# Performance work log

Measured on AMD Instinct MI355X. Metric: run time of the kernel, lower is better.

Reference implementation:

```python
import jax, jax.numpy as jnp
import numpy as np

X_DIM, R_DIM, U_DIM, V_DIM, H_DIM = 64, 64, 64, 64, 128


def setup_inputs() -> dict:
    key = jax.random.key(0)
    k1, k2, k3, k4, k5 = jax.random.split(key, 5)
    n, i, j = 8, 32, 32
    r = jax.random.normal(k1, (n, i, j, R_DIM), dtype=jnp.float32)
    u = jax.random.normal(k2, (n, R_DIM, U_DIM, V_DIM), dtype=jnp.float32)
    v = jax.random.normal(k3, (n, i, j, V_DIM), dtype=jnp.float32)
    # xavier_uniform scaling: gain=1, fan computed over last two dims per torch default
    def xavier(k, shape):
        fan_in, fan_out = shape[-1], shape[-2]
        # torch xavier on >2D tensor: fan_in = shape[1]*prod(shape[2:]), fan_out = shape[0]*prod(shape[2:])
        rf = int(np.prod(shape[2:])) if len(shape) > 2 else 1
        fi = shape[1] * rf
        fo = shape[0] * rf
        bound = float(np.sqrt(6.0 / (fi + fo)))
        return jax.random.uniform(k, shape, dtype=jnp.float32, minval=-bound, maxval=bound)
    w1 = xavier(k4, (R_DIM, U_DIM, V_DIM, H_DIM))
    w2 = xavier(k5, (X_DIM, R_DIM, H_DIM))
    return {"r": r, "u": u, "v": v, "w1": w1, "w2": w2}


def reference(r, u, v, w1, w2):
    # contract w1 with u over (u_dim, v_dim) -> per-batch tensor a[n, r, v', h]
    # original: einsum('ruvh,nruv,nijv->nijrh')
    a = jnp.einsum('ruvh,nruv->nrvh', w1, u)          # contract u axis; v survives? no:
    # Careful: in 'ruvh,nruv,nijv->nijrh', v is contracted across all three.
    # Do it in two GEMM-friendly steps: first contract u-axis, keeping v.
    # a: [n, r, v, h] (contracted only over u)
    a = jnp.einsum('ruvh,nruv->nrvh', w1, u)
    # then contract v with v-tensor: [n,i,j,v] x [n,r,v,h] -> [n,i,j,r,h]
    x = jax.nn.relu(jnp.einsum('nijv,nrvh->nijrh', v, a))
    # second einsum: 'xrh,nijr,nijrh->nijx'
    # fuse r-weighting into x first (elementwise over r), then contract (r,h) with w2
    out = jnp.einsum('xrh,nijrh->nijx', w2, x * r[..., None])
    return out
```

## Files before the change

kernel.cpp:

```cpp
#include <hip/hip_runtime.h>
#include <hip/hip_bf16.h>

#define RD 64
#define UD 64
#define VD 64
#define HD 128
#define XD 64
#define NB 8
#define SITES 1024

typedef float f32x4 __attribute__((ext_vector_type(4)));
typedef __bf16 bf16x4 __attribute__((ext_vector_type(4)));
typedef __bf16 bf16x8 __attribute__((ext_vector_type(8)));
typedef unsigned int u32x4 __attribute__((ext_vector_type(4)));
typedef unsigned short u16;
typedef unsigned short u16x4 __attribute__((ext_vector_type(4)));

__global__ void kprep(const float* __restrict__ w2, u16* __restrict__ w2t,
                      const float* __restrict__ r, float* __restrict__ rt,
                      const float* __restrict__ u, float* __restrict__ ut) {
  __shared__ float tl[64][68];
  int b = blockIdx.x;
  int t = threadIdx.x;
  if (b < 256) {
    int rr = b >> 2, qq = b & 3;
    for (int i = 0; i < 8; ++i) {
      int idx = qq * 2048 + i * 256 + t;
      int x = idx >> 7, h = idx & 127;
      float val = w2[((size_t)x * RD + rr) * HD + h];
      __hip_bfloat16 hv = __float2bfloat16(val);
      w2t[((size_t)rr * XD + x) * HD + h] = *(u16*)&hv;
    }
  } else if (b < 384) {
    int bb = b - 256;
    int n = bb >> 4, sb = (bb & 15) * 64;
    for (int i = 0; i < 4; ++i) {
      int flat = i * 256 + t;
      int s = flat >> 4, ch = flat & 15;
      f32x4 d = *(const f32x4*)(r + ((size_t)(n * SITES + sb + s) * RD + ch * 4));
      *(f32x4*)&tl[s][ch * 4] = d;
    }
    __syncthreads();
    for (int i = 0; i < 4; ++i) {
      int flat = i * 256 + t;
      int rr = flat >> 4, ch = flat & 15;
      f32x4 o;
      o.x = tl[ch * 4 + 0][rr];
      o.y = tl[ch * 4 + 1][rr];
      o.z = tl[ch * 4 + 2][rr];
      o.w = tl[ch * 4 + 3][rr];
      *(f32x4*)(rt + ((size_t)(n * RD + rr) * SITES + sb + ch * 4)) = o;
    }
  } else {
    int f = (b - 384) * 256 + t;
    int nh = f & 1, v = (f >> 1) & 63, uu = (f >> 7) & 63, rr = f >> 13;
    f32x4 o;
#pragma unroll
    for (int k = 0; k < 4; ++k)
      o[k] = u[(((size_t)(nh * 4 + k) * RD + rr) * UD + uu) * VD + v];
    *(f32x4*)(ut + (size_t)f * 4) = o;
  }
}

__global__ __launch_bounds__(256, 4) void k_a(const float* __restrict__ w1,
                                              const float* __restrict__ ut,
                                              float* __restrict__ part) {
  __shared__ float tile[32][34];
  int b = blockIdx.x;
  int rr = b >> 4, uh = (b >> 3) & 1, vh = (b >> 2) & 1, hb = b & 3;
  int t = threadIdx.x;
  int vl = t >> 3, hs = t & 7;
  int v = vh * 32 + vl;
  int h0 = hb * 32 + hs * 4;
  const float* w1p = w1 + ((size_t)((rr * UD) + uh * 32) * VD + v) * HD + h0;
  const float* up  = ut + ((size_t)((rr * UD) + uh * 32) * VD + v) * NB;

  float acc[8][4];
#pragma unroll
  for (int n = 0; n < 8; ++n)
#pragma unroll
    for (int j = 0; j < 4; ++j) acc[n][j] = 0.f;

#pragma unroll 4
  for (int uu = 0; uu < 32; ++uu) {
    f32x4 wv = *(const f32x4*)(w1p + (size_t)uu * (VD * HD));
    f32x4 a0 = *(const f32x4*)(up + (size_t)uu * (VD * NB));
    f32x4 a1 = *(const f32x4*)(up + (size_t)uu * (VD * NB) + 4);
    float un[8];
    un[0] = a0.x; un[1] = a0.y; un[2] = a0.z; un[3] = a0.w;
    un[4] = a1.x; un[5] = a1.y; un[6] = a1.z; un[7] = a1.w;
#pragma unroll
    for (int n = 0; n < 8; ++n)
#pragma unroll
      for (int j = 0; j < 4; ++j) acc[n][j] += un[n] * wv[j];
  }

  int hl = t >> 3, vs = t & 7;
  float* pb = part + (size_t)uh * (NB * RD * HD * VD);
  for (int n = 0; n < 8; ++n) {
    __syncthreads();
#pragma unroll
    for (int j = 0; j < 4; ++j) tile[hs * 4 + j][vl] = acc[n][j];
    __syncthreads();
    f32x4 blk = *(const f32x4*)&tile[hl][vs * 4];
    *(f32x4*)(pb + ((size_t)(n * RD + rr) * HD + hb * 32 + hl) * VD + vh * 32 + vs * 4) = blk;
  }
}

__global__ __launch_bounds__(256) void k_a_red(const float* __restrict__ part,
                                               u16* __restrict__ at) {
  int i0 = blockIdx.x * 256 + threadIdx.x;
  const float* p1 = part + (size_t)NB * RD * HD * VD;
#pragma unroll
  for (int k = 0; k < 4; ++k) {
    size_t i = ((size_t)i0 + (size_t)k * 262144) * 4;
    f32x4 a = *(const f32x4*)(part + i);
    f32x4 c = *(const f32x4*)(p1 + i);
    u16x4 o;
#pragma unroll
    for (int j = 0; j < 4; ++j) {
      __hip_bfloat16 hv = __float2bfloat16(a[j] + c[j]);
      o[j] = *(u16*)&hv;
    }
    *(u16x4*)(at + i) = o;
  }
}

__global__ __launch_bounds__(256, 1) void k_main(const float* __restrict__ vin,
                                                 const u16* __restrict__ at,
                                                 const u16* __restrict__ w2t,
                                                 const float* __restrict__ rt,
                                                 float* __restrict__ pbuf) {
  __shared__ __align__(16) char Plds[2 * 128 * 256];
  int b = blockIdx.x;
  int rc = b & 7, st = (b >> 3) & 7, n = b >> 6;
  int t = threadIdx.x;
  int w = t >> 6, L = t & 63, q = L >> 4, c = L & 15;
  int g1m = w >> 1, g1n = w & 1;
  int g2m = w >> 1, g2x = w & 1;

  bf16x8 vf[4][2];
#pragma unroll
  for (int nt = 0; nt < 4; ++nt)
#pragma unroll
    for (int ks = 0; ks < 2; ++ks) {
      int s = g1n * 64 + nt * 16 + c;
      const float* vp = vin + ((size_t)(n * SITES + st * 128 + s) * VD + ks * 32 + q * 8);
      f32x4 a0 = *(const f32x4*)vp;
      f32x4 a1 = *(const f32x4*)(vp + 4);
      bf16x8 f;
      f[0] = (__bf16)a0.x; f[1] = (__bf16)a0.y; f[2] = (__bf16)a0.z; f[3] = (__bf16)a0.w;
      f[4] = (__bf16)a1.x; f[5] = (__bf16)a1.y; f[6] = (__bf16)a1.z; f[7] = (__bf16)a1.w;
      vf[nt][ks] = f;
    }

  f32x4 o[4][2];
#pragma unroll
  for (int i = 0; i < 4; i++)
#pragma unroll
    for (int j = 0; j < 2; j++) o[i][j] = (f32x4)0.f;

  for (int rr = rc * 8; rr < rc * 8 + 8; ++rr) {
    const u16* abase = at + (size_t)(n * RD + rr) * 8192;

    bf16x8 af[4][2];
#pragma unroll
    for (int mt = 0; mt < 4; ++mt)
#pragma unroll
      for (int ks = 0; ks < 2; ++ks) {
        int h = g1m * 64 + mt * 16 + c;
        int vb = ks * 4 + q;
        af[mt][ks] = *(const bf16x8*)(abase + (size_t)h * VD + vb * 8);
      }
    u32x4 wraw[2][4];
#pragma unroll
    for (int xt = 0; xt < 2; ++xt)
#pragma unroll
      for (int k2 = 0; k2 < 4; ++k2) {
        int xg = g2x * 32 + xt * 16 + c;
        wraw[xt][k2] = *(const u32x4*)((const char*)w2t +
                        (((size_t)(rr * XD + xg)) * HD + k2 * 32 + q * 8) * 2);
      }
    float rsc[4];
#pragma unroll
    for (int nt = 0; nt < 4; ++nt)
      rsc[nt] = rt[(size_t)(n * RD + rr) * SITES + st * 128 + g1n * 64 + nt * 16 + c];

    f32x4 cc[4][4];
#pragma unroll
    for (int mt = 0; mt < 4; ++mt)
#pragma unroll
      for (int nt = 0; nt < 4; ++nt) cc[mt][nt] = (f32x4)0.f;
#pragma unroll
    for (int ks = 0; ks < 2; ++ks)
#pragma unroll
      for (int mt = 0; mt < 4; ++mt)
#pragma unroll
        for (int nt = 0; nt < 4; ++nt)
          cc[mt][nt] = __builtin_amdgcn_mfma_f32_16x16x32_bf16(af[mt][ks], vf[nt][ks],
                                                               cc[mt][nt], 0, 0, 0);

    char* PB = Plds + (rr & 1) * 32768;
#pragma unroll
    for (int mt = 0; mt < 4; ++mt)
#pragma unroll
      for (int nt = 0; nt < 4; ++nt) {
        float sc = rsc[nt];
        bf16x4 pv;
#pragma unroll
        for (int jj = 0; jj < 4; ++jj) {
          float x = cc[mt][nt][jj];
          x = x > 0.f ? x : 0.f;
          pv[jj] = (__bf16)(x * sc);
        }
        int s = g1n * 64 + nt * 16 + c;
        int blk = g1m * 8 + mt * 2 + (q >> 1);
        *(bf16x4*)(PB + (size_t)s * 256 + (size_t)((blk ^ c) * 16 + (q & 1) * 8)) = pv;
      }
    __syncthreads();

#pragma unroll
    for (int k2 = 0; k2 < 4; ++k2) {
      bf16x8 wf0 = __builtin_bit_cast(bf16x8, wraw[0][k2]);
      bf16x8 wf1 = __builtin_bit_cast(bf16x8, wraw[1][k2]);
#pragma unroll
      for (int mt = 0; mt < 4; ++mt) {
        int s = g2m * 64 + mt * 16 + c;
        int blk = k2 * 4 + q;
        bf16x8 pf = *(const bf16x8*)(PB + (size_t)s * 256 + (size_t)((blk ^ c) * 16));
        o[mt][0] = __builtin_amdgcn_mfma_f32_16x16x32_bf16(pf, wf0, o[mt][0], 0, 0, 0);
        o[mt][1] = __builtin_amdgcn_mfma_f32_16x16x32_bf16(pf, wf1, o[mt][1], 0, 0, 0);
      }
    }
  }
#pragma unroll
  for (int mt = 0; mt < 4; ++mt)
#pragma unroll
    for (int xt = 0; xt < 2; ++xt) {
      int s0 = g2m * 64 + mt * 16 + q * 4;
      int x = g2x * 32 + xt * 16 + c;
      size_t off = ((((size_t)rc * NB + n) * 8 + st) * XD + x) * 128 + s0;
      *(f32x4*)(pbuf + off) = o[mt][xt];
    }
}

__global__ __launch_bounds__(256) void k_reduce(const float* __restrict__ pbuf,
                                                float* __restrict__ out) {
  __shared__ float tile[128][17];
  int b = blockIdx.x;
  int n = b >> 5, st = (b >> 2) & 7, xq = b & 3;
  int t = threadIdx.x;
  int sq = t & 31, xl = t >> 5;
#pragma unroll
  for (int p = 0; p < 2; ++p) {
    int x = xq * 16 + p * 8 + xl;
    f32x4 sum = (f32x4)0.f;
#pragma unroll
    for (int rcc = 0; rcc < 8; ++rcc) {
      size_t off = ((((size_t)rcc * NB + n) * 8 + st) * XD + x) * 128 + sq * 4;
      f32x4 d = *(const f32x4*)(pbuf + off);
      sum.x += d.x; sum.y += d.y; sum.z += d.z; sum.w += d.w;
    }
#pragma unroll
    for (int k = 0; k < 4; ++k) tile[sq * 4 + k][p * 8 + xl] = sum[k];
  }
  __syncthreads();
#pragma unroll
  for (int k = 0; k < 2; ++k) {
    int flat = k * 256 + t;
    int s = flat >> 2, c4 = flat & 3;
    f32x4 o;
#pragma unroll
    for (int j = 0; j < 4; ++j) o[j] = tile[s][c4 * 4 + j];
    *(f32x4*)(out + ((size_t)(n * SITES + st * 128 + s) * XD + xq * 16 + c4 * 4)) = o;
  }
}

extern "C" void kernel_launch(void* const* d_in, const int* in_sizes, int n_in,
                              void* d_out, int out_size, void* d_ws, size_t ws_size,
                              hipStream_t stream) {
  const float* r  = (const float*)d_in[0];
  const float* u  = (const float*)d_in[1];
  const float* v  = (const float*)d_in[2];
  const float* w1 = (const float*)d_in[3];
  const float* w2 = (const float*)d_in[4];
  float* out = (float*)d_out;
  char* ws = (char*)d_ws;
  u16* at     = (u16*)(ws);
  u16* w2t    = (u16*)(ws + ((size_t)8 << 20));
  float* rt   = (float*)(ws + ((size_t)9 << 20));
  float* ut   = (float*)(ws + ((size_t)11 << 20));
  float* part = (float*)(ws + ((size_t)19 << 20));
  float* pbuf = (float*)(ws + ((size_t)51 << 20));

  hipLaunchKernelGGL(kprep, dim3(2432), dim3(256), 0, stream, w2, w2t, r, rt, u, ut);
  hipLaunchKernelGGL(k_a, dim3(1024), dim3(256), 0, stream, w1, ut, part);
  hipLaunchKernelGGL(k_a_red, dim3(1024), dim3(256), 0, stream, part, at);
  hipLaunchKernelGGL(k_main, dim3(512), dim3(256), 0, stream, v, at, w2t, rt, pbuf);
  hipLaunchKernelGGL(k_reduce, dim3(256), dim3(256), 0, stream, pbuf, out);
}
```

Measured before the change: 270.9 us.

## Drop split-U partial reduction in k_a and halve k_main site tile

```diff
diff --git a/kernel.cpp b/kernel.cpp
--- a/kernel.cpp
+++ b/kernel.cpp
@@ -14,7 +14,6 @@
 typedef __bf16 bf16x8 __attribute__((ext_vector_type(8)));
 typedef unsigned int u32x4 __attribute__((ext_vector_type(4)));
 typedef unsigned short u16;
-typedef unsigned short u16x4 __attribute__((ext_vector_type(4)));
 
 __global__ void kprep(const float* __restrict__ w2, u16* __restrict__ w2t,
                       const float* __restrict__ r, float* __restrict__ rt,
@@ -64,79 +63,61 @@
 
 __global__ __launch_bounds__(256, 4) void k_a(const float* __restrict__ w1,
                                               const float* __restrict__ ut,
-                                              float* __restrict__ part) {
-  __shared__ float tile[32][34];
-  int b = blockIdx.x;
-  int rr = b >> 4, uh = (b >> 3) & 1, vh = (b >> 2) & 1, hb = b & 3;
+                                              u16* __restrict__ at) {
+  __shared__ u16 tile[16][36];
+  int b = blockIdx.x;
+  int rr = b >> 4, vh = (b >> 3) & 1, hb = b & 7;
   int t = threadIdx.x;
   int vl = t >> 3, hs = t & 7;
   int v = vh * 32 + vl;
-  int h0 = hb * 32 + hs * 4;
-  const float* w1p = w1 + ((size_t)((rr * UD) + uh * 32) * VD + v) * HD + h0;
-  const float* up  = ut + ((size_t)((rr * UD) + uh * 32) * VD + v) * NB;
-
-  float acc[8][4];
-#pragma unroll
-  for (int n = 0; n < 8; ++n)
-#pragma unroll
-    for (int j = 0; j < 4; ++j) acc[n][j] = 0.f;
+  int h0 = hb * 16 + hs * 2;
+  const float* w1p = w1 + ((size_t)(rr * UD) * VD + v) * HD + h0;
+  const float* up  = ut + ((size_t)(rr * UD) * VD + v) * NB;
+
+  float acc[8][2];
+#pragma unroll
+  for (int n = 0; n < 8; ++n) { acc[n][0] = 0.f; acc[n][1] = 0.f; }
 
 #pragma unroll 4
-  for (int uu = 0; uu < 32; ++uu) {
-    f32x4 wv = *(const f32x4*)(w1p + (size_t)uu * (VD * HD));
+  for (int uu = 0; uu < 64; ++uu) {
+    float2 wv = *(const float2*)(w1p + (size_t)uu * (VD * HD));
     f32x4 a0 = *(const f32x4*)(up + (size_t)uu * (VD * NB));
     f32x4 a1 = *(const f32x4*)(up + (size_t)uu * (VD * NB) + 4);
     float un[8];
     un[0] = a0.x; un[1] = a0.y; un[2] = a0.z; un[3] = a0.w;
     un[4] = a1.x; un[5] = a1.y; un[6] = a1.z; un[7] = a1.w;
 #pragma unroll
-    for (int n = 0; n < 8; ++n)
-#pragma unroll
-      for (int j = 0; j < 4; ++j) acc[n][j] += un[n] * wv[j];
-  }
-
-  int hl = t >> 3, vs = t & 7;
-  float* pb = part + (size_t)uh * (NB * RD * HD * VD);
+    for (int n = 0; n < 8; ++n) {
+      acc[n][0] += un[n] * wv.x;
+      acc[n][1] += un[n] * wv.y;
+    }
+  }
+
+  int hl = t >> 4, vs = t & 15;
   for (int n = 0; n < 8; ++n) {
     __syncthreads();
 #pragma unroll
-    for (int j = 0; j < 4; ++j) tile[hs * 4 + j][vl] = acc[n][j];
-    __syncthreads();
-    f32x4 blk = *(const f32x4*)&tile[hl][vs * 4];
-    *(f32x4*)(pb + ((size_t)(n * RD + rr) * HD + hb * 32 + hl) * VD + vh * 32 + vs * 4) = blk;
-  }
-}
-
-__global__ __launch_bounds__(256) void k_a_red(const float* __restrict__ part,
-                                               u16* __restrict__ at) {
-  int i0 = blockIdx.x * 256 + threadIdx.x;
-  const float* p1 = part + (size_t)NB * RD * HD * VD;
-#pragma unroll
-  for (int k = 0; k < 4; ++k) {
-    size_t i = ((size_t)i0 + (size_t)k * 262144) * 4;
-    f32x4 a = *(const f32x4*)(part + i);
-    f32x4 c = *(const f32x4*)(p1 + i);
-    u16x4 o;
-#pragma unroll
-    for (int j = 0; j < 4; ++j) {
-      __hip_bfloat16 hv = __float2bfloat16(a[j] + c[j]);
-      o[j] = *(u16*)&hv;
-    }
-    *(u16x4*)(at + i) = o;
-  }
-}
-
-__global__ __launch_bounds__(256, 1) void k_main(const float* __restrict__ vin,
+    for (int j = 0; j < 2; ++j) {
+      __hip_bfloat16 hv = __float2bfloat16(acc[n][j]);
+      tile[hs * 2 + j][vl] = *(u16*)&hv;
+    }
+    __syncthreads();
+    unsigned int blk = *(const unsigned int*)&tile[hl][vs * 2];
+    *(unsigned int*)(at + ((size_t)(n * RD + rr) * HD + hb * 16 + hl) * VD +
+                     vh * 32 + vs * 2) = blk;
+  }
+}
+
+__global__ __launch_bounds__(256, 3) void k_main(const float* __restrict__ vin,
                                                  const u16* __restrict__ at,
                                                  const u16* __restrict__ w2t,
                                                  const float* __restrict__ rt,
                                                  float* __restrict__ pbuf) {
-  __shared__ __align__(16) char Plds[2 * 128 * 256];
-  int b = blockIdx.x;
-  int rc = b & 7, st = (b >> 3) & 7, n = b >> 6;
+  __shared__ __align__(16) char Plds[2 * 64 * 256];
+  int b = blockIdx.x;
+  int rc = b & 7, st = (b >> 3) & 15, n = b >> 7;
   int t = threadIdx.x;
   int w = t >> 6, L = t & 63, q = L >> 4, c = L & 15;
-  int g1m = w >> 1, g1n = w & 1;
   int g2m = w >> 1, g2x = w & 1;
 
   bf16x8 vf[4][2];
@@ -144,8 +125,8 @@
   for (int nt = 0; nt < 4; ++nt)
 #pragma unroll
     for (int ks = 0; ks < 2; ++ks) {
-      int s = g1n * 64 + nt * 16 + c;
-      const float* vp = vin + ((size_t)(n * SITES + st * 128 + s) * VD + ks * 32 + q * 8);
+      int s = nt * 16 + c;
+      const float* vp = vin + ((size_t)(n * SITES + st * 64 + s) * VD + ks * 32 + q * 8);
       f32x4 a0 = *(const f32x4*)vp;
       f32x4 a1 = *(const f32x4*)(vp + 4);
       bf16x8 f;
@@ -154,55 +135,55 @@
       vf[nt][ks] = f;
     }
 
-  f32x4 o[4][2];
-#pragma unroll
-  for (int i = 0; i < 4; i++)
+  f32x4 o[2][2];
+#pragma unroll
+  for (int i = 0; i < 2; i++)
 #pragma unroll
     for (int j = 0; j < 2; j++) o[i][j] = (f32x4)0.f;
 
   for (int rr = rc * 8; rr < rc * 8 + 8; ++rr) {
     const u16* abase = at + (size_t)(n * RD + rr) * 8192;
 
-    bf16x8 af[4][2];
-#pragma unroll
-    for (int mt = 0; mt < 4; ++mt)
+    bf16x8 af[2][2];
+#pragma unroll
+    for (int mt = 0; mt < 2; ++mt)
 #pragma unroll
       for (int ks = 0; ks < 2; ++ks) {
-        int h = g1m * 64 + mt * 16 + c;
+        int h = w * 32 + mt * 16 + c;
         int vb = ks * 4 + q;
         af[mt][ks] = *(const bf16x8*)(abase + (size_t)h * VD + vb * 8);
       }
     u32x4 wraw[2][4];
 #pragma unroll
-    for (int xt = 0; xt < 2; ++xt)
+    for (int nt = 0; nt < 2; ++nt)
 #pragma unroll
       for (int k2 = 0; k2 < 4; ++k2) {
-        int xg = g2x * 32 + xt * 16 + c;
-        wraw[xt][k2] = *(const u32x4*)((const char*)w2t +
+        int xg = g2x * 32 + nt * 16 + c;
+        wraw[nt][k2] = *(const u32x4*)((const char*)w2t +
                         (((size_t)(rr * XD + xg)) * HD + k2 * 32 + q * 8) * 2);
       }
     float rsc[4];
 #pragma unroll
     for (int nt = 0; nt < 4; ++nt)
-      rsc[nt] = rt[(size_t)(n * RD + rr) * SITES + st * 128 + g1n * 64 + nt * 16 + c];
-
-    f32x4 cc[4][4];
-#pragma unroll
-    for (int mt = 0; mt < 4; ++mt)
+      rsc[nt] = rt[(size_t)(n * RD + rr) * SITES + st * 64 + nt * 16 + c];
+
+    f32x4 cc[2][4];
+#pragma unroll
+    for (int mt = 0; mt < 2; ++mt)
 #pragma unroll
       for (int nt = 0; nt < 4; ++nt) cc[mt][nt] = (f32x4)0.f;
 #pragma unroll
     for (int ks = 0; ks < 2; ++ks)
 #pragma unroll
-      for (int mt = 0; mt < 4; ++mt)
+      for (int mt = 0; mt < 2; ++mt)
 #pragma unroll
         for (int nt = 0; nt < 4; ++nt)
           cc[mt][nt] = __builtin_amdgcn_mfma_f32_16x16x32_bf16(af[mt][ks], vf[nt][ks],
                                                                cc[mt][nt], 0, 0, 0);
 
-    char* PB = Plds + (rr & 1) * 32768;
-#pragma unroll
-    for (int mt = 0; mt < 4; ++mt)
+    char* PB = Plds + (rr & 1) * 16384;
+#pragma unroll
+    for (int mt = 0; mt < 2; ++mt)
 #pragma unroll
       for (int nt = 0; nt < 4; ++nt) {
         float sc = rsc[nt];
@@ -213,8 +194,8 @@
           x = x > 0.f ? x : 0.f;
           pv[jj] = (__bf16)(x * sc);
         }
-        int s = g1n * 64 + nt * 16 + c;
-        int blk = g1m * 8 + mt * 2 + (q >> 1);
+        int s = nt * 16 + c;
+        int blk = w * 4 + mt * 2 + (q >> 1);
         *(bf16x4*)(PB + (size_t)s * 256 + (size_t)((blk ^ c) * 16 + (q & 1) * 8)) = pv;
       }
     __syncthreads();
@@ -224,8 +205,8 @@
       bf16x8 wf0 = __builtin_bit_cast(bf16x8, wraw[0][k2]);
       bf16x8 wf1 = __builtin_bit_cast(bf16x8, wraw[1][k2]);
 #pragma unroll
-      for (int mt = 0; mt < 4; ++mt) {
-        int s = g2m * 64 + mt * 16 + c;
+      for (int mt = 0; mt < 2; ++mt) {
+        int s = g2m * 32 + mt * 16 + c;
         int blk = k2 * 4 + q;
         bf16x8 pf = *(const bf16x8*)(PB + (size_t)s * 256 + (size_t)((blk ^ c) * 16));
         o[mt][0] = __builtin_amdgcn_mfma_f32_16x16x32_bf16(pf, wf0, o[mt][0], 0, 0, 0);
@@ -234,45 +215,45 @@
     }
   }
 #pragma unroll
-  for (int mt = 0; mt < 4; ++mt)
-#pragma unroll
-    for (int xt = 0; xt < 2; ++xt) {
-      int s0 = g2m * 64 + mt * 16 + q * 4;
-      int x = g2x * 32 + xt * 16 + c;
-      size_t off = ((((size_t)rc * NB + n) * 8 + st) * XD + x) * 128 + s0;
-      *(f32x4*)(pbuf + off) = o[mt][xt];
+  for (int mt = 0; mt < 2; ++mt)
+#pragma unroll
+    for (int nt = 0; nt < 2; ++nt) {
+      int s0 = g2m * 32 + mt * 16 + q * 4;
+      int x = g2x * 32 + nt * 16 + c;
+      size_t off = ((((size_t)rc * NB + n) * 16 + st) * XD + x) * 64 + s0;
+      *(f32x4*)(pbuf + off) = o[mt][nt];
     }
 }
 
 __global__ __launch_bounds__(256) void k_reduce(const float* __restrict__ pbuf,
                                                 float* __restrict__ out) {
-  __shared__ float tile[128][17];
-  int b = blockIdx.x;
-  int n = b >> 5, st = (b >> 2) & 7, xq = b & 3;
-  int t = threadIdx.x;
-  int sq = t & 31, xl = t >> 5;
-#pragma unroll
-  for (int p = 0; p < 2; ++p) {
-    int x = xq * 16 + p * 8 + xl;
+  __shared__ float tile[64][68];
+  int b = blockIdx.x;
+  int n = b >> 4, st = b & 15;
+  int t = threadIdx.x;
+  int sq = t & 15, xl = t >> 4;
+#pragma unroll
+  for (int p = 0; p < 4; ++p) {
+    int x = p * 16 + xl;
     f32x4 sum = (f32x4)0.f;
 #pragma unroll
     for (int rcc = 0; rcc < 8; ++rcc) {
-      size_t off = ((((size_t)rcc * NB + n) * 8 + st) * XD + x) * 128 + sq * 4;
+      size_t off = ((((size_t)rcc * NB + n) * 16 + st) * XD + x) * 64 + sq * 4;
       f32x4 d = *(const f32x4*)(pbuf + off);
       sum.x += d.x; sum.y += d.y; sum.z += d.z; sum.w += d.w;
     }
 #pragma unroll
-    for (int k = 0; k < 4; ++k) tile[sq * 4 + k][p * 8 + xl] = sum[k];
+    for (int k = 0; k < 4; ++k) tile[sq * 4 + k][x] = sum[k];
   }
   __syncthreads();
 #pragma unroll
-  for (int k = 0; k < 2; ++k) {
+  for (int k = 0; k < 4; ++k) {
     int flat = k * 256 + t;
-    int s = flat >> 2, c4 = flat & 3;
+    int s = flat >> 4, c4 = flat & 15;
     f32x4 o;
 #pragma unroll
     for (int j = 0; j < 4; ++j) o[j] = tile[s][c4 * 4 + j];
-    *(f32x4*)(out + ((size_t)(n * SITES + st * 128 + s) * XD + xq * 16 + c4 * 4)) = o;
+    *(f32x4*)(out + ((size_t)(n * SITES + st * 64 + s) * XD + c4 * 4)) = o;
   }
 }
 
@@ -290,12 +271,10 @@
   u16* w2t    = (u16*)(ws + ((size_t)8 << 20));
   float* rt   = (float*)(ws + ((size_t)9 << 20));
   float* ut   = (float*)(ws + ((size_t)11 << 20));
-  float* part = (float*)(ws + ((size_t)19 << 20));
-  float* pbuf = (float*)(ws + ((size_t)51 << 20));
+  float* pbuf = (float*)(ws + ((size_t)19 << 20));
 
   hipLaunchKernelGGL(kprep, dim3(2432), dim3(256), 0, stream, w2, w2t, r, rt, u, ut);
-  hipLaunchKernelGGL(k_a, dim3(1024), dim3(256), 0, stream, w1, ut, part);
-  hipLaunchKernelGGL(k_a_red, dim3(1024), dim3(256), 0, stream, part, at);
-  hipLaunchKernelGGL(k_main, dim3(512), dim3(256), 0, stream, v, at, w2t, rt, pbuf);
-  hipLaunchKernelGGL(k_reduce, dim3(256), dim3(256), 0, stream, pbuf, out);
-}
+  hipLaunchKernelGGL(k_a, dim3(1024), dim3(256), 0, stream, w1, ut, at);
+  hipLaunchKernelGGL(k_main, dim3(1024), dim3(256), 0, stream, v, at, w2t, rt, pbuf);
+  hipLaunchKernelGGL(k_reduce, dim3(128), dim3(256), 0, stream, pbuf, out);
+}
```

Measured after the change: 287.2 us. 6.0% more time.

## Keep GEMM1 output in registers as GEMM2 operand via permuted w2 layout

Applied to the files above, without the earlier changes.

```diff
diff --git a/kernel.cpp b/kernel.cpp
--- a/kernel.cpp
+++ b/kernel.cpp
@@ -16,7 +16,7 @@
 typedef unsigned short u16;
 typedef unsigned short u16x4 __attribute__((ext_vector_type(4)));
 
-__global__ void kprep(const float* __restrict__ w2, u16* __restrict__ w2t,
+__global__ void kprep(const float* __restrict__ w2, u16* __restrict__ w2p,
                       const float* __restrict__ r, float* __restrict__ rt,
                       const float* __restrict__ u, float* __restrict__ ut) {
   __shared__ float tl[64][68];
@@ -26,10 +26,12 @@
     int rr = b >> 2, qq = b & 3;
     for (int i = 0; i < 8; ++i) {
       int idx = qq * 2048 + i * 256 + t;
-      int x = idx >> 7, h = idx & 127;
-      float val = w2[((size_t)x * RD + rr) * HD + h];
+      int x = idx >> 7, pos = idx & 127;
+      int k2 = pos >> 5, qd = (pos >> 3) & 3, jhi = (pos >> 2) & 1, jl = pos & 3;
+      int hsrc = k2 * 32 + jhi * 16 + qd * 4 + jl;
+      float val = w2[((size_t)x * RD + rr) * HD + hsrc];
       __hip_bfloat16 hv = __float2bfloat16(val);
-      w2t[((size_t)rr * XD + x) * HD + h] = *(u16*)&hv;
+      w2p[((size_t)rr * XD + x) * HD + pos] = *(u16*)&hv;
     }
   } else if (b < 384) {
     int bb = b - 256;
@@ -126,26 +128,23 @@
   }
 }
 
-__global__ __launch_bounds__(256, 1) void k_main(const float* __restrict__ vin,
-                                                 const u16* __restrict__ at,
-                                                 const u16* __restrict__ w2t,
-                                                 const float* __restrict__ rt,
-                                                 float* __restrict__ pbuf) {
-  __shared__ __align__(16) char Plds[2 * 128 * 256];
-  int b = blockIdx.x;
-  int rc = b & 7, st = (b >> 3) & 7, n = b >> 6;
-  int t = threadIdx.x;
-  int w = t >> 6, L = t & 63, q = L >> 4, c = L & 15;
-  int g1m = w >> 1, g1n = w & 1;
-  int g2m = w >> 1, g2x = w & 1;
-
-  bf16x8 vf[4][2];
-#pragma unroll
-  for (int nt = 0; nt < 4; ++nt)
+__global__ __launch_bounds__(64, 2) void k_main(const float* __restrict__ vin,
+                                                const u16* __restrict__ at,
+                                                const u16* __restrict__ w2p,
+                                                const float* __restrict__ rt,
+                                                float* __restrict__ pbuf) {
+  int b = blockIdx.x;
+  int stile = b & 31, rc = (b >> 5) & 7, n = b >> 8;
+  int t = threadIdx.x;
+  int q = t >> 4, c = t & 15;
+
+  bf16x8 vf[2][2];
+#pragma unroll
+  for (int nt = 0; nt < 2; ++nt)
 #pragma unroll
     for (int ks = 0; ks < 2; ++ks) {
-      int s = g1n * 64 + nt * 16 + c;
-      const float* vp = vin + ((size_t)(n * SITES + st * 128 + s) * VD + ks * 32 + q * 8);
+      const float* vp = vin + ((size_t)(n * SITES + stile * 32 + nt * 16 + c) * VD +
+                               ks * 32 + q * 8);
       f32x4 a0 = *(const f32x4*)vp;
       f32x4 a1 = *(const f32x4*)(vp + 4);
       bf16x8 f;
@@ -154,125 +153,120 @@
       vf[nt][ks] = f;
     }
 
-  f32x4 o[4][2];
-#pragma unroll
-  for (int i = 0; i < 4; i++)
-#pragma unroll
-    for (int j = 0; j < 2; j++) o[i][j] = (f32x4)0.f;
+  f32x4 o[2][4];
+#pragma unroll
+  for (int i = 0; i < 2; ++i)
+#pragma unroll
+    for (int j = 0; j < 4; ++j) o[i][j] = (f32x4)0.f;
 
   for (int rr = rc * 8; rr < rc * 8 + 8; ++rr) {
     const u16* abase = at + (size_t)(n * RD + rr) * 8192;
 
-    bf16x8 af[4][2];
-#pragma unroll
-    for (int mt = 0; mt < 4; ++mt)
-#pragma unroll
-      for (int ks = 0; ks < 2; ++ks) {
-        int h = g1m * 64 + mt * 16 + c;
-        int vb = ks * 4 + q;
-        af[mt][ks] = *(const bf16x8*)(abase + (size_t)h * VD + vb * 8);
-      }
-    u32x4 wraw[2][4];
-#pragma unroll
-    for (int xt = 0; xt < 2; ++xt)
-#pragma unroll
-      for (int k2 = 0; k2 < 4; ++k2) {
-        int xg = g2x * 32 + xt * 16 + c;
-        wraw[xt][k2] = *(const u32x4*)((const char*)w2t +
-                        (((size_t)(rr * XD + xg)) * HD + k2 * 32 + q * 8) * 2);
-      }
-    float rsc[4];
-#pragma unroll
-    for (int nt = 0; nt < 4; ++nt)
-      rsc[nt] = rt[(size_t)(n * RD + rr) * SITES + st * 128 + g1n * 64 + nt * 16 + c];
-
-    f32x4 cc[4][4];
-#pragma unroll
-    for (int mt = 0; mt < 4; ++mt)
-#pragma unroll
-      for (int nt = 0; nt < 4; ++nt) cc[mt][nt] = (f32x4)0.f;
+    bf16x8 af[8][2];
+#pragma unroll
+    for (int mt = 0; mt < 8; ++mt)
+#pragma unroll
+      for (int ks = 0; ks < 2; ++ks)
+        af[mt][ks] = *(const bf16x8*)(abase + (size_t)(mt * 16 + c) * VD +
+                                      (ks * 4 + q) * 8);
+    float rsc[2];
+#pragma unroll
+    for (int nt = 0; nt < 2; ++nt)
+      rsc[nt] = rt[(size_t)(n * RD + rr) * SITES + stile * 32 + nt * 16 + c];
+
+    f32x4 cc[8][2];
+#pragma unroll
+    for (int mt = 0; mt < 8; ++mt)
+#pragma unroll
+      for (int nt = 0; nt < 2; ++nt) cc[mt][nt] = (f32x4)0.f;
 #pragma unroll
     for (int ks = 0; ks < 2; ++ks)
 #pragma unroll
-      for (int mt = 0; mt < 4; ++mt)
-#pragma unroll
-        for (int nt = 0; nt < 4; ++nt)
+      for (int mt = 0; mt < 8; ++mt)
+#pragma unroll
+        for (int nt = 0; nt < 2; ++nt)
           cc[mt][nt] = __builtin_amdgcn_mfma_f32_16x16x32_bf16(af[mt][ks], vf[nt][ks],
                                                                cc[mt][nt], 0, 0, 0);
 
-    char* PB = Plds + (rr & 1) * 32768;
-#pragma unroll
-    for (int mt = 0; mt < 4; ++mt)
-#pragma unroll
-      for (int nt = 0; nt < 4; ++nt) {
-        float sc = rsc[nt];
-        bf16x4 pv;
+    unsigned int pw0[8][2], pw1[8][2];
+#pragma unroll
+    for (int mt = 0; mt < 8; ++mt)
+#pragma unroll
+      for (int nt = 0; nt < 2; ++nt) {
+        unsigned int w_[4];
 #pragma unroll
         for (int jj = 0; jj < 4; ++jj) {
           float x = cc[mt][nt][jj];
           x = x > 0.f ? x : 0.f;
-          pv[jj] = (__bf16)(x * sc);
+          __hip_bfloat16 hv = __float2bfloat16(x * rsc[nt]);
+          w_[jj] = *(u16*)&hv;
         }
-        int s = g1n * 64 + nt * 16 + c;
-        int blk = g1m * 8 + mt * 2 + (q >> 1);
-        *(bf16x4*)(PB + (size_t)s * 256 + (size_t)((blk ^ c) * 16 + (q & 1) * 8)) = pv;
+        pw0[mt][nt] = w_[0] | (w_[1] << 16);
+        pw1[mt][nt] = w_[2] | (w_[3] << 16);
       }
-    __syncthreads();
 
 #pragma unroll
     for (int k2 = 0; k2 < 4; ++k2) {
-      bf16x8 wf0 = __builtin_bit_cast(bf16x8, wraw[0][k2]);
-      bf16x8 wf1 = __builtin_bit_cast(bf16x8, wraw[1][k2]);
-#pragma unroll
-      for (int mt = 0; mt < 4; ++mt) {
-        int s = g2m * 64 + mt * 16 + c;
-        int blk = k2 * 4 + q;
-        bf16x8 pf = *(const bf16x8*)(PB + (size_t)s * 256 + (size_t)((blk ^ c) * 16));
-        o[mt][0] = __builtin_amdgcn_mfma_f32_16x16x32_bf16(pf, wf0, o[mt][0], 0, 0, 0);
-        o[mt][1] = __builtin_amdgcn_mfma_f32_16x16x32_bf16(pf, wf1, o[mt][1], 0, 0, 0);
+      u32x4 wk[4];
+#pragma unroll
+      for (int xt = 0; xt < 4; ++xt)
+        wk[xt] = *(const u32x4*)((const char*)w2p +
+                  (((size_t)(rr * XD + xt * 16 + c)) * HD + k2 * 32 + q * 8) * 2);
+#pragma unroll
+      for (int nt = 0; nt < 2; ++nt) {
+        u32x4 fa;
+        fa.x = pw0[2 * k2][nt];
+        fa.y = pw1[2 * k2][nt];
+        fa.z = pw0[2 * k2 + 1][nt];
+        fa.w = pw1[2 * k2 + 1][nt];
+        bf16x8 pf = __builtin_bit_cast(bf16x8, fa);
+#pragma unroll
+        for (int xt = 0; xt < 4; ++xt)
+          o[nt][xt] = __builtin_amdgcn_mfma_f32_16x16x32_bf16(
+              pf, __builtin_bit_cast(bf16x8, wk[xt]), o[nt][xt], 0, 0, 0);
       }
     }
   }
 #pragma unroll
-  for (int mt = 0; mt < 4; ++mt)
-#pragma unroll
-    for (int xt = 0; xt < 2; ++xt) {
-      int s0 = g2m * 64 + mt * 16 + q * 4;
-      int x = g2x * 32 + xt * 16 + c;
-      size_t off = ((((size_t)rc * NB + n) * 8 + st) * XD + x) * 128 + s0;
-      *(f32x4*)(pbuf + off) = o[mt][xt];
+  for (int nt = 0; nt < 2; ++nt)
+#pragma unroll
+    for (int xt = 0; xt < 4; ++xt) {
+      int sl = nt * 16 + q * 4;
+      int x = xt * 16 + c;
+      size_t off = ((((size_t)rc * NB + n) * 32 + stile) * XD + x) * 32 + sl;
+      *(f32x4*)(pbuf + off) = o[nt][xt];
     }
 }
 
 __global__ __launch_bounds__(256) void k_reduce(const float* __restrict__ pbuf,
                                                 float* __restrict__ out) {
-  __shared__ float tile[128][17];
-  int b = blockIdx.x;
-  int n = b >> 5, st = (b >> 2) & 7, xq = b & 3;
-  int t = threadIdx.x;
-  int sq = t & 31, xl = t >> 5;
+  __shared__ float tile[64][33];
+  int b = blockIdx.x;
+  int n = b >> 5, stile = b & 31;
+  int t = threadIdx.x;
 #pragma unroll
   for (int p = 0; p < 2; ++p) {
-    int x = xq * 16 + p * 8 + xl;
+    int flat = p * 256 + t;
+    int x = flat >> 3, sq = flat & 7;
     f32x4 sum = (f32x4)0.f;
 #pragma unroll
     for (int rcc = 0; rcc < 8; ++rcc) {
-      size_t off = ((((size_t)rcc * NB + n) * 8 + st) * XD + x) * 128 + sq * 4;
+      size_t off = ((((size_t)rcc * NB + n) * 32 + stile) * XD + x) * 32 + sq * 4;
       f32x4 d = *(const f32x4*)(pbuf + off);
       sum.x += d.x; sum.y += d.y; sum.z += d.z; sum.w += d.w;
     }
 #pragma unroll
-    for (int k = 0; k < 4; ++k) tile[sq * 4 + k][p * 8 + xl] = sum[k];
+    for (int k = 0; k < 4; ++k) tile[x][sq * 4 + k] = sum[k];
   }
   __syncthreads();
 #pragma unroll
-  for (int k = 0; k < 2; ++k) {
-    int flat = k * 256 + t;
-    int s = flat >> 2, c4 = flat & 3;
+  for (int p = 0; p < 2; ++p) {
+    int flat = p * 256 + t;
+    int sl = flat >> 4, xq = flat & 15;
     f32x4 o;
 #pragma unroll
-    for (int j = 0; j < 4; ++j) o[j] = tile[s][c4 * 4 + j];
-    *(f32x4*)(out + ((size_t)(n * SITES + st * 128 + s) * XD + xq * 16 + c4 * 4)) = o;
+    for (int j = 0; j < 4; ++j) o[j] = tile[xq * 4 + j][sl];
+    *(f32x4*)(out + ((size_t)(n * SITES + stile * 32 + sl) * XD + xq * 4)) = o;
   }
 }
 
@@ -287,15 +281,15 @@
   float* out = (float*)d_out;
   char* ws = (char*)d_ws;
   u16* at     = (u16*)(ws);
-  u16* w2t    = (u16*)(ws + ((size_t)8 << 20));
+  u16* w2p    = (u16*)(ws + ((size_t)8 << 20));
   float* rt   = (float*)(ws + ((size_t)9 << 20));
   float* ut   = (float*)(ws + ((size_t)11 << 20));
   float* part = (float*)(ws + ((size_t)19 << 20));
   float* pbuf = (float*)(ws + ((size_t)51 << 20));
 
-  hipLaunchKernelGGL(kprep, dim3(2432), dim3(256), 0, stream, w2, w2t, r, rt, u, ut);
+  hipLaunchKernelGGL(kprep, dim3(2432), dim3(256), 0, stream, w2, w2p, r, rt, u, ut);
   hipLaunchKernelGGL(k_a, dim3(1024), dim3(256), 0, stream, w1, ut, part);
   hipLaunchKernelGGL(k_a_red, dim3(1024), dim3(256), 0, stream, part, at);
-  hipLaunchKernelGGL(k_main, dim3(512), dim3(256), 0, stream, v, at, w2t, rt, pbuf);
+  hipLaunchKernelGGL(k_main, dim3(2048), dim3(64), 0, stream, v, at, w2p, rt, pbuf);
   hipLaunchKernelGGL(k_reduce, dim3(256), dim3(256), 0, stream, pbuf, out);
 }
```

Result: slower. 293.5 us (+8.3%).
